# Kernel optimization log

Hardware: AMD Instinct MI355X
Metric: run time of the kernel (lower is better)

The kernel has to match this reference:

```python
import jax, jax.numpy as jnp
import numpy as np
import math

B, S, H, NH = 4, 1024, 1536, 24
DH = H // NH
BUCKETS = 256          # position_buckets
MAX_REL = 512          # max_relative_positions
ATT_SPAN = BUCKETS     # pos_ebd_size
SCALE_FACTOR = 3       # 1 (content) + c2p + p2c
LN_EPS = 1e-7


def _make_log_bucket(rel, bucket_size, max_position):
    # numpy port of make_log_bucket_position (used only to build inputs)
    sign = np.sign(rel)
    mid = bucket_size // 2
    abs_pos = np.where((rel < mid) & (rel > -mid), mid - 1, np.abs(rel)).astype(np.float64)
    log_pos = np.ceil(np.log(abs_pos / mid) / np.log((max_position - 1) / mid) * (mid - 1)) + mid
    bucket = np.where(abs_pos <= mid, rel.astype(np.float64), log_pos * sign)
    return bucket.astype(np.int64)


def setup_inputs() -> dict:
    key = jax.random.key(0)
    ks = jax.random.split(key, 8)
    s = 0.02
    hidden_states = jax.random.normal(ks[0], (B, S, H), jnp.float32)
    rel_embeddings = jax.random.normal(ks[1], (2 * ATT_SPAN, H), jnp.float32)
    ids = np.arange(S)
    relative_pos = jnp.asarray(
        _make_log_bucket(ids[:, None] - ids[None, :], BUCKETS, MAX_REL)[None].astype(np.int32))  # [1,S,S]
    lengths = np.full((B,), S)
    lengths[B // 2:] = (3 * S) // 4  # some padded sequences
    valid = np.arange(S)[None, :] < lengths[:, None]  # [B,S]
    attention_mask = jnp.asarray(
        (valid[:, None, :, None] & valid[:, None, None, :]).astype(np.int32))  # [B,1,S,S]
    Wq = jax.random.normal(ks[2], (H, H), jnp.float32) * s
    Wk = jax.random.normal(ks[3], (H, H), jnp.float32) * s
    Wv = jax.random.normal(ks[4], (H, H), jnp.float32) * s
    Wo = jax.random.normal(ks[5], (H, H), jnp.float32) * s
    z = jnp.zeros((H,), jnp.float32)
    return dict(hidden_states=hidden_states, rel_embeddings=rel_embeddings,
                Wq=Wq, bq=z, Wk=Wk, bk=z, Wv=Wv, bv=z, Wo=Wo, bo=z,
                ln_g=jnp.ones((H,), jnp.float32), ln_b=z,
                attention_mask=attention_mask, relative_pos=relative_pos)


def _attention(hidden_states, rel_embeddings, Wq, bq, Wk, bk, Wv, bv, Wo, bo,
               ln_g, ln_b, attention_mask, relative_pos):
    Bm, Sm, Hm = hidden_states.shape

    def heads(x):  # [B,S,H] -> [B,NH,S,DH]
        return x.reshape(Bm, Sm, NH, DH).transpose(0, 2, 1, 3)

    q = heads(hidden_states @ Wq + bq)
    k = heads(hidden_states @ Wk + bk)
    v = heads(hidden_states @ Wv + bv)

    scale = math.sqrt(DH * SCALE_FACTOR)
    scores = jnp.einsum('bhqd,bhkd->bhqk', q, k) / scale  # content-to-content

    # share_att_key=True: reuse query/key projections on rel embeddings
    pos_k = (rel_embeddings @ Wk + bk).reshape(2 * ATT_SPAN, NH, DH).transpose(1, 0, 2)  # [NH,2P,DH]
    pos_q = (rel_embeddings @ Wq + bq).reshape(2 * ATT_SPAN, NH, DH).transpose(1, 0, 2)

    # content -> position
    c2p = jnp.einsum('bhqd,hpd->bhqp', q, pos_k)  # [B,NH,S,2P]
    c2p_idx = jnp.clip(relative_pos + ATT_SPAN, 0, 2 * ATT_SPAN - 1)[:, None]  # [1,1,S,S]
    c2p = jnp.take_along_axis(c2p, jnp.broadcast_to(c2p_idx, (Bm, NH, Sm, Sm)), axis=-1)
    scores = scores + c2p / scale

    # position -> content
    p2c = jnp.einsum('bhkd,hpd->bhkp', k, pos_q)  # [B,NH,S,2P]
    p2c_idx = jnp.clip(-relative_pos + ATT_SPAN, 0, 2 * ATT_SPAN - 1)[:, None]
    p2c = jnp.take_along_axis(p2c, jnp.broadcast_to(p2c_idx, (Bm, NH, Sm, Sm)), axis=-1)
    scores = scores + jnp.swapaxes(p2c, -1, -2) / scale

    # XSoftmax: mask==0 -> -inf before softmax, 0 after
    m = attention_mask.astype(bool)
    neg = jnp.finfo(scores.dtype).min
    probs = jax.nn.softmax(jnp.where(m, scores, neg), axis=-1)
    probs = jnp.where(m, probs, jnp.zeros((), scores.dtype))

    ctx = jnp.einsum('bhqk,bhkd->bhqd', probs, v)
    ctx = ctx.transpose(0, 2, 1, 3).reshape(Bm, Sm, Hm)

    # DebertaV2SelfOutput: dense + residual + LayerNorm
    out = ctx @ Wo + bo + hidden_states
    mu = jnp.mean(out, axis=-1, keepdims=True)
    var = jnp.mean(jnp.square(out - mu), axis=-1, keepdims=True)
    return (out - mu) / jnp.sqrt(var + LN_EPS) * ln_g + ln_b


def reference(hidden_states, rel_embeddings, Wq, bq, Wk, bk, Wv, bv, Wo, bo,
              ln_g, ln_b, attention_mask, relative_pos):
    return _attention(hidden_states, rel_embeddings, Wq, bq, Wk, bk, Wv, bv,
                      Wo, bo, ln_g, ln_b, attention_mask, relative_pos)
```

## Files before the change

kernel.cpp:

```cpp
#include <hip/hip_runtime.h>
#include <hip/hip_bf16.h>

constexpr int Bc  = 4;
constexpr int Sc  = 1024;
constexpr int Hc  = 1536;
constexpr int NHc = 24;
constexpr int P2c = 512;
constexpr int MX  = Bc * Sc;
constexpr int MA  = MX + P2c;
constexpr int N3  = 3 * Hc;
constexpr float INV_SCALE = 0.07216878364870323f;

using f32x4  = __attribute__((ext_vector_type(4))) float;
using bf16x8 = __attribute__((ext_vector_type(8))) short;
using i32x4  = __attribute__((ext_vector_type(4))) int;
using u16x8  = __attribute__((ext_vector_type(8))) unsigned short;
using u16x4  = __attribute__((ext_vector_type(4))) unsigned short;
typedef unsigned short u16;

#define DEV __device__ __forceinline__

DEV float bf2f(u16 u) { return __uint_as_float(((unsigned)u) << 16); }
DEV u16   f2bf(float f) { return __builtin_bit_cast(unsigned short, __float2bfloat16(f)); }

#if defined(__has_builtin)
#if __has_builtin(__builtin_amdgcn_global_load_lds)
#define HAVE_GLL 1
#endif
#endif
#ifndef HAVE_GLL
#define HAVE_GLL 0
#endif

DEV void stage32(u16* lds, const u16* g, int ldk, int lane) {
#pragma unroll
  for (int c = 0; c < 4; ++c) {
    const int row   = c * 8 + (lane >> 3);
    const int gslot = (lane & 7) ^ (row & 7);
    const u16* gp = g + (size_t)row * ldk + gslot * 8;
#if HAVE_GLL
    __builtin_amdgcn_global_load_lds(
        (const __attribute__((address_space(1))) void*)gp,
        (__attribute__((address_space(3))) void*)(lds + c * 8 * 64),
        16, 0, 0);
#else
    i32x4 v = *(const i32x4*)gp;
    *(i32x4*)(lds + row * 64 + (lane & 7) * 8) = v;
#endif
  }
}

DEV bf16x8 ldsFrag(const u16* base, int row, int kh, int lhi) {
  const int idx = row * 64 + ((kh * 32 + lhi * 8) ^ ((row & 7) * 8));
  return *(const bf16x8*)(base + idx);
}

template <int MODE>
__global__ __launch_bounds__(256) void gemm128(
    const u16* __restrict__ A, const u16* __restrict__ Bt,
    const float* __restrict__ bias, const float* __restrict__ resid,
    u16* __restrict__ outb, float* __restrict__ outf, int ldo)
{
  __shared__ alignas(16) u16 As[128 * 64];
  __shared__ alignas(16) u16 Bs[128 * 64];
  const int tid = threadIdx.x, wid = tid >> 6, lane = tid & 63;
  const int wr = wid >> 1, wc = wid & 1;
  const int l15 = lane & 15, lhi = lane >> 4;
  const int m0 = blockIdx.y * 128, n0 = blockIdx.x * 128;

  f32x4 acc[4][4] = {};
#pragma unroll 1
  for (int kt = 0; kt < 24; ++kt) {
    const int k0 = kt * 64;
    stage32(As + wid * (32 * 64), A  + (size_t)(m0 + wid * 32) * 1536 + k0, 1536, lane);
    stage32(Bs + wid * (32 * 64), Bt + (size_t)(n0 + wid * 32) * 1536 + k0, 1536, lane);
    asm volatile("s_waitcnt vmcnt(0)" ::: "memory");
    __syncthreads();
#pragma unroll
    for (int kh = 0; kh < 2; ++kh) {
      bf16x8 af[4], bfv[4];
#pragma unroll
      for (int mt = 0; mt < 4; ++mt) af[mt]  = ldsFrag(As, wr * 64 + mt * 16 + l15, kh, lhi);
#pragma unroll
      for (int nt = 0; nt < 4; ++nt) bfv[nt] = ldsFrag(Bs, wc * 64 + nt * 16 + l15, kh, lhi);
#pragma unroll
      for (int mt = 0; mt < 4; ++mt)
#pragma unroll
        for (int nt = 0; nt < 4; ++nt)
          acc[mt][nt] = __builtin_amdgcn_mfma_f32_16x16x32_bf16(af[mt], bfv[nt], acc[mt][nt], 0, 0, 0);
    }
    __syncthreads();
  }
#pragma unroll
  for (int mt = 0; mt < 4; ++mt)
#pragma unroll
    for (int nt = 0; nt < 4; ++nt) {
      const int gn = n0 + wc * 64 + nt * 16 + l15;
      const float bs = bias[gn];
#pragma unroll
      for (int r = 0; r < 4; ++r) {
        const int gm = m0 + wr * 64 + mt * 16 + lhi * 4 + r;
        float v = acc[mt][nt][r] + bs;
        if (MODE == 0) {
          if (gn < Hc) v *= INV_SCALE;
          outb[(size_t)gm * ldo + gn] = f2bf(v);
        } else {
          v += resid[(size_t)gm * ldo + gn];
          outf[(size_t)gm * ldo + gn] = v;
        }
      }
    }
}

__global__ __launch_bounds__(256) void prep_misc(
    const float* __restrict__ bq, const float* __restrict__ bk, const float* __restrict__ bv,
    const int* __restrict__ am, const int* __restrict__ rp,
    float* __restrict__ bias, int* __restrict__ valid, u16* __restrict__ tbl)
{
  const int TOT = N3 + MX + 2047;
  for (int i = blockIdx.x * 256 + threadIdx.x; i < TOT; i += gridDim.x * 256) {
    if (i < N3) {
      bias[i] = i < Hc ? bq[i] : (i < 2 * Hc ? bk[i - Hc] : bv[i - 2 * Hc]);
    } else if (i < N3 + MX) {
      const int j = i - N3, b = j >> 10, s = j & 1023;
      valid[j] = am[(size_t)b * Sc * Sc + (size_t)s * Sc + s];
    } else {
      const int t = i - (N3 + MX), d = t - 1023;
      int v = (d >= 0 ? rp[(size_t)d * Sc] : rp[-d]) + 256;
      v = v < 0 ? 0 : (v > 511 ? 511 : v);
      tbl[t] = (u16)v;
    }
  }
}

__global__ void len_kernel(const int* __restrict__ valid, int* __restrict__ LENS)
{
  const int tid = threadIdx.x, wid = tid >> 6, lane = tid & 63;
  int s = 0;
#pragma unroll
  for (int j = 0; j < 16; ++j) s += valid[wid * Sc + j * 64 + lane];
#pragma unroll
  for (int off = 1; off <= 32; off <<= 1) s += __shfl_xor(s, off);
  if (lane == 0) LENS[wid] = s;
}

__global__ __launch_bounds__(256) void cast_x(const float* __restrict__ hs,
                                              const float* __restrict__ rel,
                                              u16* __restrict__ A)
{
  const size_t total = (size_t)MA * Hc / 4;
  for (size_t i = (size_t)blockIdx.x * 256 + threadIdx.x; i < total; i += (size_t)gridDim.x * 256) {
    const size_t e = i * 4;
    const int row = (int)(e / Hc), col = (int)(e % Hc);
    const float* s = row < MX ? hs + (size_t)row * Hc + col : rel + (size_t)(row - MX) * Hc + col;
    f32x4 v = *(const f32x4*)s;
    u16x4 o = { f2bf(v[0]), f2bf(v[1]), f2bf(v[2]), f2bf(v[3]) };
    *(u16x4*)(A + e) = o;
  }
}

__global__ void transpose_cast(const float* __restrict__ Wq, const float* __restrict__ Wk,
                               const float* __restrict__ Wv, const float* __restrict__ Wo,
                               u16* __restrict__ WT, u16* __restrict__ WOT)
{
  const int z = blockIdx.z;
  const float* src = z == 0 ? Wq : z == 1 ? Wk : z == 2 ? Wv : Wo;
  u16* dst = z == 3 ? WOT : WT + (size_t)z * Hc * Hc;
  __shared__ float t[32][33];
  const int tx = threadIdx.x, ty = threadIdx.y;
  const int kb = blockIdx.y * 32, nb = blockIdx.x * 32;
#pragma unroll
  for (int i = 0; i < 4; ++i)
    t[ty + i * 8][tx] = src[(size_t)(kb + ty + i * 8) * Hc + nb + tx];
  __syncthreads();
#pragma unroll
  for (int i = 0; i < 4; ++i)
    dst[(size_t)(nb + ty + i * 8) * Hc + kb + tx] = f2bf(t[tx][ty + i * 8]);
}

__global__ __launch_bounds__(256) void relmat4(const u16* __restrict__ QKVP,
    u16* __restrict__ c2p, u16* __restrict__ p2cT, const int* __restrict__ LENS, int bh_base)
{
  const int lbh = blockIdx.x >> 3, v = blockIdx.x & 7;
  const int bh = bh_base + lbh, b = bh / NHc, h = bh % NHc;
  const int tid = threadIdx.x, wid = tid >> 6, lane = tid & 63;
  const int l15 = lane & 15, lhi = lane >> 4, lhi4 = lhi * 4;

  __shared__ alignas(16) u16 Bs[512 * 64];

  int m0, n0, ldo;
  size_t arow, brow;
  u16* out;
  if (v < 4) {
    m0 = v * 256; n0 = 0; ldo = P2c;
    if (m0 >= LENS[b]) return;
    arow = (size_t)b * Sc + m0; brow = (size_t)MX;
    out = c2p + (size_t)lbh * Sc * P2c;
  } else {
    m0 = ((v - 4) >> 1) * 256; n0 = ((v - 4) & 1) * 512; ldo = Sc;
    arow = (size_t)MX + m0; brow = (size_t)b * Sc + n0;
    out = p2cT + (size_t)lbh * P2c * Sc;
  }
  const int acol = h * 64;
  const int bcol = Hc + h * 64;

  const int srow = tid >> 3;
  const int gsl  = (tid & 7) ^ (srow & 7);
#pragma unroll
  for (int it = 0; it < 16; ++it) {
    const int row = it * 32 + srow;
    const u16* gp = QKVP + (brow + row) * 4608 + bcol + gsl * 8;
#if HAVE_GLL
    __builtin_amdgcn_global_load_lds(
        (const __attribute__((address_space(1))) void*)gp,
        (__attribute__((address_space(3))) void*)(&Bs[it * 2048 + wid * 512]),
        16, 0, 0);
#else
    *(i32x4*)(&Bs[row * 64 + (tid & 7) * 8]) = *(const i32x4*)gp;
#endif
  }

  bf16x8 af[4][2];
#pragma unroll
  for (int mt = 0; mt < 4; ++mt)
#pragma unroll
    for (int kh = 0; kh < 2; ++kh)
      af[mt][kh] = *(const bf16x8*)(QKVP + (arow + wid * 64 + mt * 16 + l15) * 4608
                                    + acol + kh * 32 + lhi * 8);

  asm volatile("s_waitcnt vmcnt(0)" ::: "memory");
  __syncthreads();

#pragma unroll 4
  for (int nt = 0; nt < 32; ++nt) {
    bf16x8 b0 = ldsFrag(Bs, nt * 16 + l15, 0, lhi);
    bf16x8 b1 = ldsFrag(Bs, nt * 16 + l15, 1, lhi);
    f32x4 acc[4] = {};
#pragma unroll
    for (int mt = 0; mt < 4; ++mt) {
      acc[mt] = __builtin_amdgcn_mfma_f32_16x16x32_bf16(af[mt][0], b0, acc[mt], 0, 0, 0);
      acc[mt] = __builtin_amdgcn_mfma_f32_16x16x32_bf16(af[mt][1], b1, acc[mt], 0, 0, 0);
    }
#pragma unroll
    for (int mt = 0; mt < 4; ++mt)
#pragma unroll
      for (int r = 0; r < 4; ++r) {
        const int mm = m0 + wid * 64 + mt * 16 + lhi4 + r;
        const int nn = n0 + nt * 16 + l15;
        out[(size_t)mm * ldo + nn] = f2bf(acc[mt][r]);
      }
  }
}

DEV int svz(int d) { return ((d ^ (d >> 3)) & 7) << 3; }

__global__ __launch_bounds__(256) void flash8(
    const u16* __restrict__ QKVP, const u16* __restrict__ c2p, const u16* __restrict__ p2cT,
    const int* __restrict__ LENS, const u16* __restrict__ tblG,
    u16* __restrict__ ctx, int bh_base, int chunkC)
{
  int id = blockIdx.x;
  const int grid = chunkC * 16;
  if ((grid & 7) == 0) { const int cpx = grid >> 3; id = (id & 7) * cpx + (id >> 3); }
  const int lbh = id >> 4, qi = id & 15;
  const int bh = bh_base + lbh, b = bh / NHc, h = bh % NHc;
  const int q0 = qi * 64;
  const int tid = threadIdx.x, wid = tid >> 6, lane = tid & 63;
  const int l15 = lane & 15, lhi = lane >> 4, lhi4 = lhi * 4;
  const int qrb = q0 + wid * 16;
  const int len = LENS[b];

  if (q0 >= len) {
    u16x8 z = {};
#pragma unroll
    for (int i = 0; i < 2; ++i) {
      const int t = i * 256 + tid;
      *(u16x8*)(ctx + (size_t)(b * Sc + q0 + (t >> 3)) * Hc + h * 64 + (t & 7) * 8) = z;
    }
    return;
  }
  const int nkt = (len + 63) >> 6;

  __shared__ u16 Tt[2048];
  __shared__ alignas(16) u16 cWs[64 * 152];
  __shared__ alignas(16) u16 pWs[136 * 68];
  __shared__ alignas(16) u16 Kt[64 * 64];
  __shared__ alignas(16) u16 Vt[64 * 64];
  __shared__ alignas(16) u16 Pl[4][16 * 64];

  const u16* c2pB  = c2p  + (size_t)lbh * Sc * P2c;
  const u16* p2cTB = p2cT + (size_t)lbh * P2c * Sc;
  const u16* Qg = QKVP + (size_t)b * Sc * 4608 + h * 64;
  const u16* Kg = QKVP + (size_t)b * Sc * 4608 + Hc + h * 64;
  const u16* Vg = QKVP + (size_t)b * Sc * 4608 + 2 * Hc + h * 64;

  for (int i = tid; i < 2047; i += 256) Tt[i] = tblG[i];

  bf16x8 aq[2];
#pragma unroll
  for (int kh = 0; kh < 2; ++kh)
    aq[kh] = *(const bf16x8*)(Qg + (size_t)(qrb + l15) * 4608 + kh * 32 + lhi * 8);

  const int kr = tid >> 2, dc = (tid & 3) * 16;
  const int sk = (kr & 7) * 8;

  u16x8 rcw[5], rpw[5], rk0, rk1, rv0, rv1;

  auto issue = [&](int k0, int c0a) {
#pragma unroll
    for (int i = 0; i < 5; ++i) {
      const int s = i * 256 + tid;
      if (s < 1152) {
        const int row = s / 18, ch = s - row * 18;
        rcw[i] = *(const u16x8*)(c2pB + (size_t)(q0 + row) * P2c + c0a + ch * 8);
      }
    }
#pragma unroll
    for (int i = 0; i < 5; ++i) {
      const int s = i * 256 + tid;
      if (s < 1088) {
        const int row = s >> 3, ch = s & 7;
        rpw[i] = *(const u16x8*)(p2cTB + (size_t)(c0a + row) * Sc + k0 + ch * 8);
      }
    }
    const size_t ro = (size_t)(k0 + kr) * 4608 + dc;
    rk0 = *(const u16x8*)(Kg + ro); rk1 = *(const u16x8*)(Kg + ro + 8);
    rv0 = *(const u16x8*)(Vg + ro); rv1 = *(const u16x8*)(Vg + ro + 8);
  };

  auto commit = [&]() {
#pragma unroll
    for (int i = 0; i < 5; ++i) {
      const int s = i * 256 + tid;
      if (s < 1152) {
        const int row = s / 18, ch = s - row * 18;
        *(u16x8*)(cWs + row * 152 + ch * 8) = rcw[i];
      }
    }
#pragma unroll
    for (int i = 0; i < 5; ++i) {
      const int s = i * 256 + tid;
      if (s < 1088) {
        const int row = s >> 3, ch = s & 7;
        u16x4 lo = { rpw[i][0], rpw[i][1], rpw[i][2], rpw[i][3] };
        u16x4 hi = { rpw[i][4], rpw[i][5], rpw[i][6], rpw[i][7] };
        *(u16x4*)(pWs + row * 68 + ch * 8)     = lo;
        *(u16x4*)(pWs + row * 68 + ch * 8 + 4) = hi;
      }
    }
    *(u16x8*)(Kt + kr * 64 + (dc ^ sk))       = rk0;
    *(u16x8*)(Kt + kr * 64 + ((dc ^ sk) ^ 8)) = rk1;
#pragma unroll
    for (int i = 0; i < 8; ++i) { const int d = dc + i;     Vt[d * 64 + (kr ^ svz(d))] = rv0[i]; }
#pragma unroll
    for (int i = 0; i < 8; ++i) { const int d = dc + 8 + i; Vt[d * 64 + (kr ^ svz(d))] = rv1[i]; }
  };

  __syncthreads();
  int cc0a = Tt[q0 + 960] & ~7;
  issue(0, cc0a);
  asm volatile("s_waitcnt vmcnt(0)" ::: "memory");
  commit();
  __syncthreads();

  u16* myP = Pl[wid];
  f32x4 o_acc[4] = {};
  float lsum[4] = { 0.f, 0.f, 0.f, 0.f };
  int cc0a_n = 0;

  for (int kt = 0; kt < nkt; ++kt) {
    const int k0 = kt * 64;
    const bool more = (kt + 1 < nkt);
    if (more) {
      cc0a_n = Tt[q0 - (k0 + 64) - 63 + 1023] & ~7;
      issue(k0 + 64, cc0a_n);
    }

    f32x4 s[4];
    __builtin_amdgcn_s_setprio(1);
#pragma unroll
    for (int j = 0; j < 4; ++j) {
      f32x4 sv = {};
#pragma unroll
      for (int kh = 0; kh < 2; ++kh) {
        bf16x8 bk = ldsFrag(Kt, j * 16 + l15, kh, lhi);
        sv = __builtin_amdgcn_mfma_f32_16x16x32_bf16(aq[kh], bk, sv, 0, 0, 0);
      }
      s[j] = sv;
    }
    __builtin_amdgcn_s_setprio(0);

    float p[4][4];
#pragma unroll
    for (int j = 0; j < 4; ++j) {
      const int kloc = j * 16 + l15;
      const bool kvld = (k0 + kloc) < len;
#pragma unroll
      for (int r = 0; r < 4; ++r) {
        const int q = qrb + lhi4 + r;
        const int w = Tt[q - (k0 + kloc) + 1023] - cc0a;
        const float rel = bf2f(cWs[(wid * 16 + lhi4 + r) * 152 + w])
                        + bf2f(pWs[w * 68 + kloc]);
        p[j][r] = kvld ? __expf(s[j][r] + rel) : 0.f;
      }
    }
#pragma unroll
    for (int r = 0; r < 4; ++r)
      lsum[r] += (p[0][r] + p[1][r]) + (p[2][r] + p[3][r]);

#pragma unroll
    for (int j = 0; j < 4; ++j)
#pragma unroll
      for (int r = 0; r < 4; ++r) {
        const int row = lhi4 + r, col = j * 16 + l15;
        myP[row * 64 + (col ^ ((row & 7) * 8))] = f2bf(p[j][r]);
      }

    __builtin_amdgcn_s_setprio(1);
#pragma unroll
    for (int kh = 0; kh < 2; ++kh) {
      bf16x8 pa = *(const bf16x8*)(myP + l15 * 64 + ((kh * 32 + lhi * 8) ^ ((l15 & 7) * 8)));
#pragma unroll
      for (int jd = 0; jd < 4; ++jd) {
        const int d = jd * 16 + l15;
        bf16x8 vf = *(const bf16x8*)(Vt + d * 64 + ((kh * 32 + lhi * 8) ^ svz(d)));
        o_acc[jd] = __builtin_amdgcn_mfma_f32_16x16x32_bf16(pa, vf, o_acc[jd], 0, 0, 0);
      }
    }
    __builtin_amdgcn_s_setprio(0);

    __syncthreads();
    if (more) {
      asm volatile("s_waitcnt vmcnt(0)" ::: "memory");
      commit();
      cc0a = cc0a_n;
    }
    __syncthreads();
  }

#pragma unroll
  for (int r = 0; r < 4; ++r) {
    float l = lsum[r];
#pragma unroll
    for (int off = 1; off <= 8; off <<= 1) l += __shfl_xor(l, off);
    const int q = qrb + lhi4 + r;
    const float inv = (q < len && l > 0.f) ? 1.f / l : 0.f;
#pragma unroll
    for (int jd = 0; jd < 4; ++jd)
      ctx[(size_t)(b * Sc + q) * Hc + h * 64 + jd * 16 + l15] = f2bf(o_acc[jd][r] * inv);
  }
}

__global__ __launch_bounds__(256) void ln_kernel(float* __restrict__ io,
    const float* __restrict__ g, const float* __restrict__ bta)
{
  const int row = blockIdx.x;
  float* p = io + (size_t)row * Hc;
  const int tid = threadIdx.x, wid = tid >> 6, lane = tid & 63;
  float v[6];
  float s = 0.f;
#pragma unroll
  for (int j = 0; j < 6; ++j) { v[j] = p[tid + j * 256]; s += v[j]; }
#pragma unroll
  for (int off = 1; off <= 32; off <<= 1) s += __shfl_xor(s, off);
  __shared__ float red[4];
  if (lane == 0) red[wid] = s;
  __syncthreads();
  const float mu = (red[0] + red[1] + red[2] + red[3]) * (1.f / Hc);
  float q = 0.f;
#pragma unroll
  for (int j = 0; j < 6; ++j) { const float d = v[j] - mu; q += d * d; }
#pragma unroll
  for (int off = 1; off <= 32; off <<= 1) q += __shfl_xor(q, off);
  __syncthreads();
  if (lane == 0) red[wid] = q;
  __syncthreads();
  const float rstd = rsqrtf((red[0] + red[1] + red[2] + red[3]) * (1.f / Hc) + 1e-7f);
#pragma unroll
  for (int j = 0; j < 6; ++j) {
    const int c = tid + j * 256;
    p[c] = (v[j] - mu) * rstd * g[c] + bta[c];
  }
}

extern "C" void kernel_launch(void* const* d_in, const int* in_sizes, int n_in,
                              void* d_out, int out_size, void* d_ws, size_t ws_size,
                              hipStream_t stream)
{
  (void)in_sizes; (void)n_in; (void)out_size;
  const float* hidden = (const float*)d_in[0];
  const float* relemb = (const float*)d_in[1];
  const float* Wq = (const float*)d_in[2];
  const float* bq = (const float*)d_in[3];
  const float* Wk = (const float*)d_in[4];
  const float* bk = (const float*)d_in[5];
  const float* Wv = (const float*)d_in[6];
  const float* bv = (const float*)d_in[7];
  const float* Wo = (const float*)d_in[8];
  const float* bo = (const float*)d_in[9];
  const float* lng = (const float*)d_in[10];
  const float* lnb = (const float*)d_in[11];
  const int* am = (const int*)d_in[12];
  const int* rp = (const int*)d_in[13];
  float* out = (float*)d_out;

  char* ws = (char*)d_ws;
  size_t off = 0;
  auto alloc = [&](size_t bytes) { size_t r = off; off += (bytes + 255) & ~(size_t)255; return r; };
  const size_t o_qkvp = alloc((size_t)MA * 4608 * 2);
  const size_t o_wt   = alloc((size_t)N3 * Hc * 2);
  const size_t o_wot  = alloc((size_t)Hc * Hc * 2);
  const size_t o_abig = alloc((size_t)MA * Hc * 2);
  const size_t o_bias = alloc((size_t)N3 * 4);
  const size_t o_valid= alloc((size_t)MX * 4);
  const size_t o_tbl  = alloc(2048 * 2);
  const size_t o_lens = alloc(256);
  const size_t fixed  = off;
  const size_t o_rel  = off;

  const size_t perbh = (size_t)Sc * P2c * 2 * 2;
  const size_t guard = 512 * 1024;
  int c = 96;
  while (c > 1 && fixed + (size_t)c * perbh + guard > ws_size) c >>= 1;

  u16* QKVP = (u16*)(ws + o_qkvp);
  u16* WT   = (u16*)(ws + o_wt);
  u16* WOT  = (u16*)(ws + o_wot);
  u16* ABIG = (u16*)(ws + o_abig);
  u16* CTX  = (u16*)(ws + o_abig);
  float* BIAS = (float*)(ws + o_bias);
  int* VALID  = (int*)(ws + o_valid);
  u16* TBL  = (u16*)(ws + o_tbl);
  int* LENS = (int*)(ws + o_lens);
  u16* C2P  = (u16*)(ws + o_rel);
  u16* P2CT = C2P + (size_t)c * Sc * P2c;

  prep_misc<<<dim3(50), dim3(256), 0, stream>>>(bq, bk, bv, am, rp, BIAS, VALID, TBL);
  len_kernel<<<dim3(1), dim3(256), 0, stream>>>(VALID, LENS);
  cast_x<<<dim3(1728), dim3(256), 0, stream>>>(hidden, relemb, ABIG);
  transpose_cast<<<dim3(48, 48, 4), dim3(32, 8), 0, stream>>>(Wq, Wk, Wv, Wo, WT, WOT);
  gemm128<0><<<dim3(36, 36), dim3(256), 0, stream>>>(ABIG, WT, BIAS, (const float*)nullptr,
                                                     QKVP, (float*)nullptr, 4608);
  for (int base = 0; base < 96; base += c) {
    relmat4<<<dim3(8 * c), dim3(256), 0, stream>>>(QKVP, C2P, P2CT, LENS, base);
    flash8<<<dim3(c * 16), dim3(256), 0, stream>>>(QKVP, C2P, P2CT, LENS, TBL, CTX, base, c);
  }
  gemm128<1><<<dim3(12, 32), dim3(256), 0, stream>>>(CTX, WOT, bo, hidden,
                                                     (u16*)nullptr, out, Hc);
  ln_kernel<<<dim3(MX), dim3(256), 0, stream>>>(out, lng, lnb);
}
```

Measured before the change: 392.1 us.

## Pre-transpose V globally, pack bucket table pairs, merge prep kernels

Adds a separate kernel that writes V transposed per head, so the flash kernel can store V tiles to LDS with vectorized writes instead of scalar scattered stores. The relative-bucket table is packed as adjacent pairs in 32-bit words, which cuts LDS table lookups in the softmax inner loop. The length computation is folded into the prep kernel, removing one launch and the valid buffer. In exchange it adds an extra kernel pass and extra workspace for the transposed V.

```diff
diff --git a/kernel.cpp b/kernel.cpp
--- a/kernel.cpp
+++ b/kernel.cpp
@@ -17,6 +17,7 @@
 using u16x8  = __attribute__((ext_vector_type(8))) unsigned short;
 using u16x4  = __attribute__((ext_vector_type(4))) unsigned short;
 typedef unsigned short u16;
+typedef unsigned int u32;
 
 #define DEV __device__ __forceinline__
 
@@ -112,36 +113,40 @@
     }
 }
 
-__global__ __launch_bounds__(256) void prep_misc(
+__global__ __launch_bounds__(256) void prep2(
     const float* __restrict__ bq, const float* __restrict__ bk, const float* __restrict__ bv,
     const int* __restrict__ am, const int* __restrict__ rp,
-    float* __restrict__ bias, int* __restrict__ valid, u16* __restrict__ tbl)
-{
-  const int TOT = N3 + MX + 2047;
+    float* __restrict__ bias, u32* __restrict__ TBL2, int* __restrict__ LENS)
+{
+  const int TOT = N3 + 2048;
   for (int i = blockIdx.x * 256 + threadIdx.x; i < TOT; i += gridDim.x * 256) {
     if (i < N3) {
       bias[i] = i < Hc ? bq[i] : (i < 2 * Hc ? bk[i - Hc] : bv[i - 2 * Hc]);
-    } else if (i < N3 + MX) {
-      const int j = i - N3, b = j >> 10, s = j & 1023;
-      valid[j] = am[(size_t)b * Sc * Sc + (size_t)s * Sc + s];
     } else {
-      const int t = i - (N3 + MX), d = t - 1023;
-      int v = (d >= 0 ? rp[(size_t)d * Sc] : rp[-d]) + 256;
-      v = v < 0 ? 0 : (v > 511 ? 511 : v);
-      tbl[t] = (u16)v;
-    }
-  }
-}
-
-__global__ void len_kernel(const int* __restrict__ valid, int* __restrict__ LENS)
-{
-  const int tid = threadIdx.x, wid = tid >> 6, lane = tid & 63;
-  int s = 0;
-#pragma unroll
-  for (int j = 0; j < 16; ++j) s += valid[wid * Sc + j * 64 + lane];
-#pragma unroll
-  for (int off = 1; off <= 32; off <<= 1) s += __shfl_xor(s, off);
-  if (lane == 0) LENS[wid] = s;
+      const int t = i - N3;
+      auto Tf = [&](int tt) -> u32 {
+        tt = tt > 2046 ? 2046 : tt;
+        const int d = tt - 1023;
+        int v = (d >= 0 ? rp[(size_t)d * Sc] : rp[-d]) + 256;
+        return (u32)(v < 0 ? 0 : (v > 511 ? 511 : v));
+      };
+      TBL2[t] = Tf(t) | (Tf(t + 1) << 16);
+    }
+  }
+  if (blockIdx.x == 0) {
+    const int wid = threadIdx.x >> 6, lane = threadIdx.x & 63;
+    if (wid < 4) {
+      int s = 0;
+#pragma unroll
+      for (int j = 0; j < 16; ++j) {
+        const int ss = j * 64 + lane;
+        s += am[(size_t)wid * Sc * Sc + (size_t)ss * Sc + ss] != 0;
+      }
+#pragma unroll
+      for (int off = 1; off <= 32; off <<= 1) s += __shfl_xor(s, off);
+      if (lane == 0) LENS[wid] = s;
+    }
+  }
 }
 
 __global__ __launch_bounds__(256) void cast_x(const float* __restrict__ hs,
@@ -176,6 +181,26 @@
 #pragma unroll
   for (int i = 0; i < 4; ++i)
     dst[(size_t)(nb + ty + i * 8) * Hc + kb + tx] = f2bf(t[tx][ty + i * 8]);
+}
+
+__global__ __launch_bounds__(256) void vt_kernel(const u16* __restrict__ QKVP,
+                                                 u16* __restrict__ VT)
+{
+  const int kt = blockIdx.x, bh = blockIdx.y, b = bh / NHc, h = bh % NHc;
+  __shared__ u16 t[64][72];
+  const int row = threadIdx.x >> 2, c4 = (threadIdx.x & 3) * 16;
+  const u16* Vg = QKVP + (size_t)(b * Sc + kt * 64 + row) * 4608 + 2 * Hc + h * 64 + c4;
+  u16x8 a0 = *(const u16x8*)Vg, a1 = *(const u16x8*)(Vg + 8);
+#pragma unroll
+  for (int i = 0; i < 8; ++i) t[c4 + i][row] = a0[i];
+#pragma unroll
+  for (int i = 0; i < 8; ++i) t[c4 + 8 + i][row] = a1[i];
+  __syncthreads();
+  u16x8 o0 = *(const u16x8*)(&t[row][c4]);
+  u16x8 o1 = *(const u16x8*)(&t[row][c4 + 8]);
+  u16* dst = VT + ((size_t)bh * 64 + row) * Sc + kt * 64 + c4;
+  *(u16x8*)dst = o0;
+  *(u16x8*)(dst + 8) = o1;
 }
 
 __global__ __launch_bounds__(256) void relmat4(const u16* __restrict__ QKVP,
@@ -254,9 +279,10 @@
 
 DEV int svz(int d) { return ((d ^ (d >> 3)) & 7) << 3; }
 
-__global__ __launch_bounds__(256) void flash8(
-    const u16* __restrict__ QKVP, const u16* __restrict__ c2p, const u16* __restrict__ p2cT,
-    const int* __restrict__ LENS, const u16* __restrict__ tblG,
+__global__ __launch_bounds__(256) void flash9(
+    const u16* __restrict__ QKVP, const u16* __restrict__ VT,
+    const u16* __restrict__ c2p, const u16* __restrict__ p2cT,
+    const int* __restrict__ LENS, const u32* __restrict__ TBL2g,
     u16* __restrict__ ctx, int bh_base, int chunkC)
 {
   int id = blockIdx.x;
@@ -281,7 +307,7 @@
   }
   const int nkt = (len + 63) >> 6;
 
-  __shared__ u16 Tt[2048];
+  __shared__ u32 Lt2[2048];
   __shared__ alignas(16) u16 cWs[64 * 152];
   __shared__ alignas(16) u16 pWs[136 * 68];
   __shared__ alignas(16) u16 Kt[64 * 64];
@@ -290,11 +316,11 @@
 
   const u16* c2pB  = c2p  + (size_t)lbh * Sc * P2c;
   const u16* p2cTB = p2cT + (size_t)lbh * P2c * Sc;
-  const u16* Qg = QKVP + (size_t)b * Sc * 4608 + h * 64;
-  const u16* Kg = QKVP + (size_t)b * Sc * 4608 + Hc + h * 64;
-  const u16* Vg = QKVP + (size_t)b * Sc * 4608 + 2 * Hc + h * 64;
-
-  for (int i = tid; i < 2047; i += 256) Tt[i] = tblG[i];
+  const u16* Qg  = QKVP + (size_t)b * Sc * 4608 + h * 64;
+  const u16* Kg  = QKVP + (size_t)b * Sc * 4608 + Hc + h * 64;
+  const u16* VTg = VT + (size_t)bh * 64 * Sc;
+
+  for (int i = tid; i < 2048; i += 256) Lt2[i] = TBL2g[i];
 
   bf16x8 aq[2];
 #pragma unroll
@@ -325,7 +351,8 @@
     }
     const size_t ro = (size_t)(k0 + kr) * 4608 + dc;
     rk0 = *(const u16x8*)(Kg + ro); rk1 = *(const u16x8*)(Kg + ro + 8);
-    rv0 = *(const u16x8*)(Vg + ro); rv1 = *(const u16x8*)(Vg + ro + 8);
+    const u16* vp = VTg + (size_t)kr * Sc + k0 + dc;
+    rv0 = *(const u16x8*)vp; rv1 = *(const u16x8*)(vp + 8);
   };
 
   auto commit = [&]() {
@@ -350,14 +377,12 @@
     }
     *(u16x8*)(Kt + kr * 64 + (dc ^ sk))       = rk0;
     *(u16x8*)(Kt + kr * 64 + ((dc ^ sk) ^ 8)) = rk1;
-#pragma unroll
-    for (int i = 0; i < 8; ++i) { const int d = dc + i;     Vt[d * 64 + (kr ^ svz(d))] = rv0[i]; }
-#pragma unroll
-    for (int i = 0; i < 8; ++i) { const int d = dc + 8 + i; Vt[d * 64 + (kr ^ svz(d))] = rv1[i]; }
+    *(u16x8*)(Vt + kr * 64 + (dc ^ sk))       = rv0;
+    *(u16x8*)(Vt + kr * 64 + ((dc ^ sk) ^ 8)) = rv1;
   };
 
   __syncthreads();
-  int cc0a = Tt[q0 + 960] & ~7;
+  int cc0a = (int)(Lt2[q0 + 960] & 0xFFFF) & ~7;
   issue(0, cc0a);
   asm volatile("s_waitcnt vmcnt(0)" ::: "memory");
   commit();
@@ -372,7 +397,7 @@
     const int k0 = kt * 64;
     const bool more = (kt + 1 < nkt);
     if (more) {
-      cc0a_n = Tt[q0 - (k0 + 64) - 63 + 1023] & ~7;
+      cc0a_n = (int)(Lt2[q0 - (k0 + 64) - 63 + 1023] & 0xFFFF) & ~7;
       issue(k0 + 64, cc0a_n);
     }
 
@@ -395,12 +420,15 @@
     for (int j = 0; j < 4; ++j) {
       const int kloc = j * 16 + l15;
       const bool kvld = (k0 + kloc) < len;
+      const int t0 = qrb + lhi4 - (k0 + kloc) + 1023;
+      const u32 wA = Lt2[t0], wB = Lt2[t0 + 2];
+      const int ccr0 = (int)(wA & 0xFFFF), ccr1 = (int)(wA >> 16);
+      const int ccr2 = (int)(wB & 0xFFFF), ccr3 = (int)(wB >> 16);
+      const int wv[4] = { ccr0 - cc0a, ccr1 - cc0a, ccr2 - cc0a, ccr3 - cc0a };
 #pragma unroll
       for (int r = 0; r < 4; ++r) {
-        const int q = qrb + lhi4 + r;
-        const int w = Tt[q - (k0 + kloc) + 1023] - cc0a;
-        const float rel = bf2f(cWs[(wid * 16 + lhi4 + r) * 152 + w])
-                        + bf2f(pWs[w * 68 + kloc]);
+        const float rel = bf2f(cWs[(wid * 16 + lhi4 + r) * 152 + wv[r]])
+                        + bf2f(pWs[wv[r] * 68 + kloc]);
         p[j][r] = kvld ? __expf(s[j][r] + rel) : 0.f;
       }
     }
@@ -422,8 +450,7 @@
       bf16x8 pa = *(const bf16x8*)(myP + l15 * 64 + ((kh * 32 + lhi * 8) ^ ((l15 & 7) * 8)));
 #pragma unroll
       for (int jd = 0; jd < 4; ++jd) {
-        const int d = jd * 16 + l15;
-        bf16x8 vf = *(const bf16x8*)(Vt + d * 64 + ((kh * 32 + lhi * 8) ^ svz(d)));
+        bf16x8 vf = ldsFrag(Vt, jd * 16 + l15, kh, lhi);
         o_acc[jd] = __builtin_amdgcn_mfma_f32_16x16x32_bf16(pa, vf, o_acc[jd], 0, 0, 0);
       }
     }
@@ -511,9 +538,9 @@
   const size_t o_wt   = alloc((size_t)N3 * Hc * 2);
   const size_t o_wot  = alloc((size_t)Hc * Hc * 2);
   const size_t o_abig = alloc((size_t)MA * Hc * 2);
+  const size_t o_vt   = alloc((size_t)96 * 64 * Sc * 2);
   const size_t o_bias = alloc((size_t)N3 * 4);
-  const size_t o_valid= alloc((size_t)MX * 4);
-  const size_t o_tbl  = alloc(2048 * 2);
+  const size_t o_tbl2 = alloc(2048 * 4);
   const size_t o_lens = alloc(256);
   const size_t fixed  = off;
   const size_t o_rel  = off;
@@ -528,22 +555,23 @@
   u16* WOT  = (u16*)(ws + o_wot);
   u16* ABIG = (u16*)(ws + o_abig);
   u16* CTX  = (u16*)(ws + o_abig);
+  u16* VT   = (u16*)(ws + o_vt);
   float* BIAS = (float*)(ws + o_bias);
-  int* VALID  = (int*)(ws + o_valid);
-  u16* TBL  = (u16*)(ws + o_tbl);
+  u32* TBL2 = (u32*)(ws + o_tbl2);
   int* LENS = (int*)(ws + o_lens);
   u16* C2P  = (u16*)(ws + o_rel);
   u16* P2CT = C2P + (size_t)c * Sc * P2c;
 
-  prep_misc<<<dim3(50), dim3(256), 0, stream>>>(bq, bk, bv, am, rp, BIAS, VALID, TBL);
-  len_kernel<<<dim3(1), dim3(256), 0, stream>>>(VALID, LENS);
+  prep2<<<dim3(26), dim3(256), 0, stream>>>(bq, bk, bv, am, rp, BIAS, TBL2, LENS);
   cast_x<<<dim3(1728), dim3(256), 0, stream>>>(hidden, relemb, ABIG);
   transpose_cast<<<dim3(48, 48, 4), dim3(32, 8), 0, stream>>>(Wq, Wk, Wv, Wo, WT, WOT);
   gemm128<0><<<dim3(36, 36), dim3(256), 0, stream>>>(ABIG, WT, BIAS, (const float*)nullptr,
                                                      QKVP, (float*)nullptr, 4608);
+  vt_kernel<<<dim3(16, 96), dim3(256), 0, stream>>>(QKVP, VT);
   for (int base = 0; base < 96; base += c) {
     relmat4<<<dim3(8 * c), dim3(256), 0, stream>>>(QKVP, C2P, P2CT, LENS, base);
-    flash8<<<dim3(c * 16), dim3(256), 0, stream>>>(QKVP, C2P, P2CT, LENS, TBL, CTX, base, c);
+    flash9<<<dim3(c * 16), dim3(256), 0, stream>>>(QKVP, VT, C2P, P2CT, LENS, TBL2,
+                                                   CTX, base, c);
   }
   gemm128<1><<<dim3(12, 32), dim3(256), 0, stream>>>(CTX, WOT, bo, hidden,
                                                      (u16*)nullptr, out, Hc);
```

New measurement: 389.2 us. Within noise of the previous version (-0.7%).
